# Kernel tuning notes

Hardware: AMD Instinct MI355X
Metric: run time of the kernel (lower is better)

Reference implementation:

```python
import jax, jax.numpy as jnp
import numpy as np

HEADS = 12
DIM_HEAD = 64
INNER = HEADS * DIM_HEAD  # 768
DIM = 512
KS = 3


def setup_inputs() -> dict:
    key = jax.random.key(0)
    ks = jax.random.split(key, 5)
    B, H, W = 8, 32, 32
    N = H * W + 1  # +1 cls token -> has_cls path
    x = jax.random.normal(ks[0], (B, N, DIM), dtype=jnp.float32)
    w_qkv = jax.random.normal(ks[1], (3 * INNER, DIM), dtype=jnp.float32) * (DIM ** -0.5)
    w_dw = jax.random.normal(ks[2], (DIM, 1, KS, KS), dtype=jnp.float32) * (1.0 / KS)
    w_out = jax.random.normal(ks[3], (DIM, INNER), dtype=jnp.float32) * (INNER ** -0.5)
    b_out = jax.random.normal(ks[4], (DIM,), dtype=jnp.float32) * 0.01
    return {"x": x, "w_qkv": w_qkv, "w_dw": w_dw, "w_out": w_out,
            "b_out": b_out, "h_feat": H, "w_feat": W}


def reference(x, w_qkv, w_dw, w_out, b_out, h_feat, w_feat):
    B, N, C = x.shape
    scale = DIM_HEAD ** -0.5
    # qkv projection (Linear, no bias): torch weight layout (out,in)
    qkv = jnp.einsum('bnc,oc->bno', x, w_qkv)  # (B,N,3*INNER)
    q, k, v = jnp.split(qkv, 3, axis=-1)

    def split_heads(t):
        return t.reshape(B, N, HEADS, DIM_HEAD).transpose(0, 2, 1, 3)  # (B,H,N,d)

    q, k, v = map(split_heads, (q, k, v))
    dots = jnp.einsum('bhid,bhjd->bhij', q, k) * scale
    attn = jax.nn.softmax(dots, axis=-1)
    out_attn = jnp.einsum('bhij,bhjd->bhid', attn, v)
    out_attn = out_attn.transpose(0, 2, 1, 3).reshape(B, N, INNER)

    has_cls = (N == h_feat * w_feat + 1)  # static
    spatial = x[:, 1:, :] if has_cls else x
    spatial_2d = spatial.transpose(0, 2, 1).reshape(B, C, h_feat, w_feat)
    # depthwise conv, padding = ks//2 (SAME for odd ks, stride 1)
    loc = jax.lax.conv_general_dilated(
        spatial_2d, w_dw, window_strides=(1, 1), padding='SAME',
        feature_group_count=C,
        dimension_numbers=('NCHW', 'OIHW', 'NCHW'))
    local_out = loc.reshape(B, C, h_feat * w_feat).transpose(0, 2, 1)  # (B,hw,C)
    if has_cls:
        cls_out = x[:, :1, :INNER]  # C < INNER so this is the full cls token
        local_out = jnp.concatenate([cls_out, local_out], axis=1)  # (B,N,C)
    if local_out.shape[-1] < INNER:
        out = out_attn + jnp.pad(
            local_out, ((0, 0), (0, 0), (0, INNER - local_out.shape[-1])))
    else:
        out = out_attn
    # output Linear (dropout=0 in eval)
    return jnp.einsum('bni,oi->bno', out, w_out) + b_out
```

## Files before the change

### kernel.cpp

```cpp
#include <hip/hip_runtime.h>
#include <hip/hip_bf16.h>
#include <stdint.h>
#include <math.h>

typedef __bf16 bf16;
typedef __bf16 bf16x8 __attribute__((ext_vector_type(8)));
typedef float f32x4 __attribute__((ext_vector_type(4)));

#define QSCALE 0.1803368801111f


__device__ __forceinline__ void gload_lds16(const void* g, void* l) {
  typedef const __attribute__((address_space(1))) char g_char;
  typedef __attribute__((address_space(3))) char l_char;
  g_char* gp = (g_char*)(uintptr_t)g;
  l_char* lp = (l_char*)(uint32_t)(uintptr_t)l;
  __builtin_amdgcn_global_load_lds(gp, lp, 16, 0, 0);
}

__device__ __forceinline__ float fexp2(float x) {
#if __has_builtin(__builtin_amdgcn_exp2f)
  return __builtin_amdgcn_exp2f(x);
#else
  return exp2f(x);
#endif
}

__device__ __forceinline__ float frcp(float x) {
#if __has_builtin(__builtin_amdgcn_rcpf)
  return __builtin_amdgcn_rcpf(x);
#else
  return 1.f / x;
#endif
}

__device__ __forceinline__ uint32_t pk2(float a, float b) {
  union { bf16 h; unsigned short u; } ua, ub;
  ua.h = (bf16)a; ub.h = (bf16)b;
  return (uint32_t)ua.u | ((uint32_t)ub.u << 16);
}

__global__ __launch_bounds__(256) void k_prep(const float* __restrict__ x,
                                              const float* __restrict__ wqkv,
                                              const float* __restrict__ wout,
                                              bf16* __restrict__ xb, bf16* __restrict__ wqkvb,
                                              bf16* __restrict__ woutb, bf16* __restrict__ vT) {
  int i = blockIdx.x * 256 + threadIdx.x;
  const float* src = nullptr;
  bf16* dst = nullptr;
  int q = i;
  bool zero = false;
  if (i < 1064960) {
    if (i < 1049600) src = x; else zero = true;
    dst = xb;
  } else if (i < 1064960 + 294912) {
    q = i - 1064960; src = wqkv; dst = wqkvb;
  } else if (i < 1064960 + 294912 + 98304) {
    q = i - (1064960 + 294912); src = wout; dst = woutb;
  } else {
    int qq = i - (1064960 + 294912 + 98304);
    int e = qq * 4;
    int rd = e >> 6;
    int n = 1024 + (e & 63);
    uint2 z; z.x = 0u; z.y = 0u;
    *(uint2*)&vT[(size_t)rd * 1088 + n] = z;
    return;
  }
  float4 v = make_float4(0.f, 0.f, 0.f, 0.f);
  if (!zero) v = *(const float4*)&src[(size_t)q * 4];
  uint2 p;
  p.x = pk2(v.x, v.y);
  p.y = pk2(v.z, v.w);
  *(uint2*)&dst[(size_t)q * 4] = p;
}

template <int EPI, int BN>
__global__ __launch_bounds__(256) void k_gemm(const bf16* __restrict__ A,
                                              const bf16* __restrict__ Bt, int K,
                                              bf16* __restrict__ q, bf16* __restrict__ kk,
                                              bf16* __restrict__ vt,
                                              const float* __restrict__ bias,
                                              float* __restrict__ out) {
  __shared__ __attribute__((aligned(16))) bf16 sA[128 * 64];
  __shared__ __attribute__((aligned(16))) bf16 sB[BN * 64];
  constexpr int MF = (BN == 128) ? 4 : 2;
  constexpr int WROWS = (BN == 128) ? 64 : 32;
  const int tid = threadIdx.x;
  const int lane = tid & 63;
  const int w = tid >> 6;
  const int wr = (BN == 128) ? (w >> 1) : w;
  const int wc = (BN == 128) ? (w & 1) : 0;
  const int tn = blockIdx.x, tm = blockIdx.y;
  const int l15 = lane & 15, l4 = lane >> 4;
  const int srow = lane >> 3, sslot = lane & 7;

  f32x4 acc[MF][4] = {};

  const int Ksteps = K >> 6;
  for (int kt = 0; kt < Ksteps; ++kt) {
    __syncthreads();
#pragma unroll
    for (int i = 0; i < 4; ++i) {
      int row = w * 32 + i * 8 + srow;
      int clog = sslot ^ (row & 7);
      gload_lds16(A + ((size_t)(tm * 128 + row) * K + kt * 64 + clog * 8),
                  &sA[(w * 32 + i * 8) * 64]);
    }
#pragma unroll
    for (int i = 0; i < BN / 32; ++i) {
      int row = w * (BN / 4) + i * 8 + srow;
      int clog = sslot ^ (row & 7);
      gload_lds16(Bt + ((size_t)(tn * BN + row) * K + kt * 64 + clog * 8),
                  &sB[(w * (BN / 4) + i * 8) * 64]);
    }
    __syncthreads();
#pragma unroll
    for (int ks = 0; ks < 2; ++ks) {
      bf16x8 af[MF], bfr[4];
#pragma unroll
      for (int mf = 0; mf < MF; ++mf) {
        int row = wr * WROWS + mf * 16 + l15;
        int phys = (ks * 4 + l4) ^ (row & 7);
        af[mf] = *(const bf16x8*)&sA[row * 64 + phys * 8];
      }
#pragma unroll
      for (int nf = 0; nf < 4; ++nf) {
        int row = wc * 64 + nf * 16 + l15;
        int phys = (ks * 4 + l4) ^ (row & 7);
        bfr[nf] = *(const bf16x8*)&sB[row * 64 + phys * 8];
      }
#pragma unroll
      for (int mf = 0; mf < MF; ++mf)
#pragma unroll
        for (int nf = 0; nf < 4; ++nf)
          acc[mf][nf] =
              __builtin_amdgcn_mfma_f32_16x16x32_bf16(af[mf], bfr[nf], acc[mf][nf], 0, 0, 0);
    }
  }

  const int Rbase = tm * 128 + wr * WROWS + l4 * 4;
  const int Cbase = tn * BN + wc * 64 + l15;
#pragma unroll
  for (int mf = 0; mf < MF; ++mf) {
    int R0 = Rbase + mf * 16;
    if (R0 >= 8200) continue;
    if (EPI == 0) {
      int b = R0 / 1025;
      int n0 = R0 - b * 1025;
      bool sb = (n0 + 3 <= 1024);
#pragma unroll
      for (int nf = 0; nf < 4; ++nf) {
        int Cc = Cbase + nf * 16;
        int seg = (Cc >= 1536) ? 2 : (Cc >= 768 ? 1 : 0);
        int inner = Cc - seg * 768;
        int h = inner >> 6, d = inner & 63;
        if (seg == 2) {
          if (sb) {
            uint2 p;
            p.x = pk2(acc[mf][nf][0], acc[mf][nf][1]);
            p.y = pk2(acc[mf][nf][2], acc[mf][nf][3]);
            *(uint2*)&vt[(((size_t)b * 12 + h) * 64 + d) * 1088 + n0] = p;
          } else {
#pragma unroll
            for (int r = 0; r < 4; ++r) {
              int R = R0 + r;
              int b2 = R / 1025;
              int n = R - b2 * 1025;
              vt[(((size_t)b2 * 12 + h) * 64 + d) * 1088 + n] = (bf16)acc[mf][nf][r];
            }
          }
        } else {
          bf16* dst = seg ? kk : q;
          float scl = seg ? 1.f : QSCALE;
#pragma unroll
          for (int r = 0; r < 4; ++r) {
            int b2, n;
            if (sb) { b2 = b; n = n0 + r; }
            else { int R = R0 + r; b2 = R / 1025; n = R - b2 * 1025; }
            dst[(((size_t)b2 * 12 + h) * 1088 + n) * 64 + d] = (bf16)(acc[mf][nf][r] * scl);
          }
        }
      }
    } else {
#pragma unroll
      for (int r = 0; r < 4; ++r) {
        int R = R0 + r;
#pragma unroll
        for (int nf = 0; nf < 4; ++nf) {
          int Cc = Cbase + nf * 16;
          out[(size_t)R * 512 + Cc] = acc[mf][nf][r] + bias[Cc];
        }
      }
    }
  }
}

__global__ __launch_bounds__(256) void k_flash(const bf16* __restrict__ qg,
                                               const bf16* __restrict__ kg,
                                               const bf16* __restrict__ vtg,
                                               bf16* __restrict__ outb) {
  __shared__ __attribute__((aligned(16))) bf16 sK[2][64 * 64];
  __shared__ __attribute__((aligned(16))) bf16 sV[2][64 * 64];
  __shared__ __attribute__((aligned(16))) bf16 sP[4][16 * 64];
  const int tid = threadIdx.x, lane = tid & 63, w = tid >> 6;
  const int l15 = lane & 15, l4 = lane >> 4;
  const int wg = blockIdx.x;
  const int logical = (wg & 7) * 108 + (wg >> 3);
  const int bh = logical / 9, qgp = logical - bh * 9;
  const int b = bh / 12, h = bh - b * 12;
  const int srow = lane >> 3, sslot = lane & 7;
  const int nsub = (qgp == 8) ? 1 : 2;
  const int swz = (l15 & 7) << 3;

  bf16x8 qf[2][2];
#pragma unroll
  for (int s = 0; s < 2; ++s) {
    if (s < nsub) {
      size_t qoff = ((size_t)bh * 1088 + (qgp * 2 + s) * 64 + w * 16 + l15) * 64 + l4 * 8;
      qf[s][0] = *(const bf16x8*)&qg[qoff];
      qf[s][1] = *(const bf16x8*)&qg[qoff + 32];
    }
  }

  float mreg[2] = {-INFINITY, -INFINITY};
  float lreg[2] = {0.f, 0.f};
  f32x4 oa[2][4] = {};

  const int px0 = (l4 ^ (l15 & 7)) * 8;
  const int px1 = ((4 + l4) ^ (l15 & 7)) * 8;
  const int stRow = (w * 16 + srow) * 64;
  const int stRow2 = (w * 16 + 8 + srow) * 64;

  auto STAGE = [&](int bi, int t) {
    int row = w * 16 + srow;
    int clog = sslot ^ (row & 7);
    gload_lds16(kg + ((size_t)bh * 1088 + t * 64 + row) * 64 + clog * 8, &sK[bi][stRow]);
    gload_lds16(vtg + ((size_t)bh * 64 + row) * 1088 + t * 64 + clog * 8, &sV[bi][stRow]);
    int row2 = row + 8;
    int clog2 = sslot ^ (row2 & 7);
    gload_lds16(kg + ((size_t)bh * 1088 + t * 64 + row2) * 64 + clog2 * 8, &sK[bi][stRow2]);
    gload_lds16(vtg + ((size_t)bh * 64 + row2) * 1088 + t * 64 + clog2 * 8, &sV[bi][stRow2]);
  };

  STAGE(0, 0);
  int cur = 0;

  for (int t = 0; t < 17; ++t) {
    asm volatile("s_waitcnt vmcnt(0)" ::: "memory");
    __builtin_amdgcn_s_barrier();
    __builtin_amdgcn_sched_barrier(0);
    if (t < 16) STAGE(cur ^ 1, t + 1);

    const bf16* kb_ = sK[cur];
    const bf16* vb_ = sV[cur];

    bf16x8 af[2][4], vf[2][4];
#pragma unroll
    for (int jt = 0; jt < 4; ++jt) {
      af[0][jt] = *(const bf16x8*)&kb_[(jt * 16 + l15) * 64 + px0];
      af[1][jt] = *(const bf16x8*)&kb_[(jt * 16 + l15) * 64 + px1];
      vf[0][jt] = *(const bf16x8*)&vb_[(jt * 16 + l15) * 64 + px0];
      vf[1][jt] = *(const bf16x8*)&vb_[(jt * 16 + l15) * 64 + px1];
    }

#pragma unroll
    for (int s = 0; s < 2; ++s) {
      if (s >= nsub) continue;
      f32x4 sc[4] = {};
      __builtin_amdgcn_s_setprio(1);
#pragma unroll
      for (int ks = 0; ks < 2; ++ks)
#pragma unroll
        for (int jt = 0; jt < 4; ++jt)
          sc[jt] = __builtin_amdgcn_mfma_f32_16x16x32_bf16(af[ks][jt], qf[s][ks], sc[jt], 0, 0, 0);
      __builtin_amdgcn_s_setprio(0);

      if (t == 16) {
#pragma unroll
        for (int jt = 0; jt < 4; ++jt)
#pragma unroll
          for (int r = 0; r < 4; ++r) {
            if (jt == 0 && r == 0)
              sc[jt][r] = (l4 == 0) ? sc[jt][r] : -INFINITY;
            else
              sc[jt][r] = -INFINITY;
          }
      }

      float pm = fmaxf(fmaxf(fmaxf(sc[0][0], sc[0][1]), fmaxf(sc[0][2], sc[0][3])),
                       fmaxf(fmaxf(sc[1][0], sc[1][1]), fmaxf(sc[1][2], sc[1][3])));
      float pm2 = fmaxf(fmaxf(fmaxf(sc[2][0], sc[2][1]), fmaxf(sc[2][2], sc[2][3])),
                        fmaxf(fmaxf(sc[3][0], sc[3][1]), fmaxf(sc[3][2], sc[3][3])));
      pm = fmaxf(pm, pm2);
      pm = fmaxf(pm, __shfl_xor(pm, 16));
      pm = fmaxf(pm, __shfl_xor(pm, 32));

      if (__any(pm > mreg[s] + 8.0f)) {
        float mn = fmaxf(mreg[s], pm);
        float alpha = fexp2(mreg[s] - mn);
        mreg[s] = mn;
        lreg[s] *= alpha;
        float ar[4];
#pragma unroll
        for (int r = 0; r < 4; ++r) ar[r] = __shfl(alpha, l4 * 4 + r);
#pragma unroll
        for (int db = 0; db < 4; ++db)
#pragma unroll
          for (int r = 0; r < 4; ++r) oa[s][db][r] *= ar[r];
      }
      float mn = mreg[s];

      float rs = 0.f;
#pragma unroll
      for (int jt = 0; jt < 4; ++jt) {
        float p0 = fexp2(sc[jt][0] - mn);
        float p1 = fexp2(sc[jt][1] - mn);
        float p2 = fexp2(sc[jt][2] - mn);
        float p3 = fexp2(sc[jt][3] - mn);
        rs += (p0 + p1) + (p2 + p3);
        uint2 pkd;
        pkd.x = pk2(p0, p1);
        pkd.y = pk2(p2, p3);
        *(uint2*)&sP[w][l15 * 64 + ((jt * 16 + l4 * 4) ^ swz)] = pkd;
      }
      rs += __shfl_xor(rs, 16);
      rs += __shfl_xor(rs, 32);
      lreg[s] += rs;

      __builtin_amdgcn_s_setprio(1);
#pragma unroll
      for (int ks = 0; ks < 2; ++ks) {
        bf16x8 pf = *(const bf16x8*)&sP[w][l15 * 64 + ((ks * 32 + l4 * 8) ^ swz)];
#pragma unroll
        for (int db = 0; db < 4; ++db)
          oa[s][db] = __builtin_amdgcn_mfma_f32_16x16x32_bf16(pf, vf[ks][db], oa[s][db], 0, 0, 0);
      }
      __builtin_amdgcn_s_setprio(0);
    }
    cur ^= 1;
  }

#pragma unroll
  for (int s = 0; s < 2; ++s) {
    if (s >= nsub) continue;
    float linv = frcp(lreg[s]);
#pragma unroll
    for (int r = 0; r < 4; ++r) {
      float ir = __shfl(linv, l4 * 4 + r);
      int n = (qgp * 2 + s) * 64 + w * 16 + l4 * 4 + r;
      if (n >= 1025) continue;
#pragma unroll
      for (int db = 0; db < 4; ++db)
        outb[((size_t)b * 1025 + n) * 768 + h * 64 + db * 16 + l15] = (bf16)(oa[s][db][r] * ir);
    }
  }
}

__global__ __launch_bounds__(256) void k_local(const float* __restrict__ x,
                                               const float* __restrict__ wdw,
                                               bf16* __restrict__ outb) {
  const int b = blockIdx.x, y = blockIdx.y, xseg = blockIdx.z, c0 = threadIdx.x;
  const int x0 = xseg * 8;
  const bool hm = (y > 0), hp = (y < 31);
#pragma unroll
  for (int hf = 0; hf < 2; ++hf) {
    const int c = hf * 256 + c0;
    float w9[9];
#pragma unroll
    for (int k = 0; k < 9; ++k) w9[k] = wdw[(size_t)c * 9 + k];
    const float* xb = x + ((size_t)b * 1025 + 1) * 512 + c;
    float A = 0.f, Bp = 0.f;
    for (int cc = x0 - 1; cc <= x0 + 8; ++cc) {
      float v0 = 0.f, v1 = 0.f, v2 = 0.f;
      if (cc >= 0 && cc < 32) {
        v1 = xb[((size_t)y * 32 + cc) * 512];
        if (hm) v0 = xb[((size_t)(y - 1) * 32 + cc) * 512];
        if (hp) v2 = xb[((size_t)(y + 1) * 32 + cc) * 512];
      }
      float t0 = v0 * w9[0] + v1 * w9[3] + v2 * w9[6];
      float t1 = v0 * w9[1] + v1 * w9[4] + v2 * w9[7];
      float t2 = v0 * w9[2] + v1 * w9[5] + v2 * w9[8];
      int oc = cc - 1;
      if (oc >= x0 && oc <= x0 + 7) {
        float acc = A + t2;
        size_t o = ((size_t)b * 1025 + 1 + y * 32 + oc) * 768 + c;
        outb[o] = (bf16)((float)outb[o] + acc);
      }
      A = Bp + t1;
      Bp = t0;
    }
  }
  if (y == 0 && xseg == 0) {
#pragma unroll
    for (int hf = 0; hf < 2; ++hf) {
      int c = hf * 256 + c0;
      size_t o = ((size_t)b * 1025) * 768 + c;
      outb[o] = (bf16)((float)outb[o] + x[((size_t)b * 1025) * 512 + c]);
    }
  }
}

extern "C" void kernel_launch(void* const* d_in, const int* in_sizes, int n_in,
                              void* d_out, int out_size, void* d_ws, size_t ws_size,
                              hipStream_t stream) {
  const float* x = (const float*)d_in[0];
  const float* w_qkv = (const float*)d_in[1];
  const float* w_dw = (const float*)d_in[2];
  const float* w_out = (const float*)d_in[3];
  const float* b_out = (const float*)d_in[4];
  float* out = (float*)d_out;

  char* ws = (char*)d_ws;
  size_t off = 0;
  auto alloc = [&](size_t bytes) {
    char* p = ws + off;
    off = (off + bytes + 255) & ~(size_t)255;
    return p;
  };
  bf16* xb    = (bf16*)alloc((size_t)8320 * 512 * 2);
  bf16* wqkvb = (bf16*)alloc((size_t)2304 * 512 * 2);
  bf16* woutb = (bf16*)alloc((size_t)512 * 768 * 2);
  bf16* qb    = (bf16*)alloc((size_t)96 * 1088 * 64 * 2);
  bf16* kb    = (bf16*)alloc((size_t)96 * 1088 * 64 * 2);
  bf16* vT    = (bf16*)alloc((size_t)96 * 64 * 1088 * 2);
  bf16* outb  = (bf16*)alloc((size_t)8320 * 768 * 2);

  k_prep<<<6080, 256, 0, stream>>>(x, w_qkv, w_out, xb, wqkvb, woutb, vT);
  k_gemm<0, 128><<<dim3(18, 65), 256, 0, stream>>>(xb, wqkvb, 512, qb, kb, vT, nullptr, nullptr);
  k_flash<<<864, 256, 0, stream>>>(qb, kb, vT, outb);
  k_local<<<dim3(8, 32, 4), 256, 0, stream>>>(x, w_dw, outb);
  k_gemm<1, 64><<<dim3(8, 65), 256, 0, stream>>>(outb, woutb, 768, nullptr, nullptr, nullptr,
                                                 b_out, out);
}
```

Baseline: 160.3 us.

## Redistribute softmax probabilities via lane shuffles instead of LDS round-trip

```diff
diff --git a/kernel.cpp b/kernel.cpp
--- a/kernel.cpp
+++ b/kernel.cpp
@@ -201,7 +201,6 @@
                                                bf16* __restrict__ outb) {
   __shared__ __attribute__((aligned(16))) bf16 sK[2][64 * 64];
   __shared__ __attribute__((aligned(16))) bf16 sV[2][64 * 64];
-  __shared__ __attribute__((aligned(16))) bf16 sP[4][16 * 64];
   const int tid = threadIdx.x, lane = tid & 63, w = tid >> 6;
   const int l15 = lane & 15, l4 = lane >> 4;
   const int wg = blockIdx.x;
@@ -210,7 +209,7 @@
   const int b = bh / 12, h = bh - b * 12;
   const int srow = lane >> 3, sslot = lane & 7;
   const int nsub = (qgp == 8) ? 1 : 2;
-  const int swz = (l15 & 7) << 3;
+  const int aa = l4 >> 1, bb = l4 & 1;
 
   bf16x8 qf[2][2];
 #pragma unroll
@@ -310,31 +309,49 @@
       }
       float mn = mreg[s];
 
-      float rs = 0.f;
-#pragma unroll
-      for (int jt = 0; jt < 4; ++jt) {
-        float p0 = fexp2(sc[jt][0] - mn);
-        float p1 = fexp2(sc[jt][1] - mn);
-        float p2 = fexp2(sc[jt][2] - mn);
-        float p3 = fexp2(sc[jt][3] - mn);
-        rs += (p0 + p1) + (p2 + p3);
-        uint2 pkd;
-        pkd.x = pk2(p0, p1);
-        pkd.y = pk2(p2, p3);
-        *(uint2*)&sP[w][l15 * 64 + ((jt * 16 + l4 * 4) ^ swz)] = pkd;
-      }
-      rs += __shfl_xor(rs, 16);
-      rs += __shfl_xor(rs, 32);
-      lreg[s] += rs;
+      uint32_t pk0u0, pk0u1, pk1u0, pk1u1, pk2u0, pk2u1, pk3u0, pk3u1;
+      float lsum = 0.f;
+      {
+        float p0, p1, p2, p3;
+        p0 = fexp2(sc[0][0] - mn); p1 = fexp2(sc[0][1] - mn);
+        p2 = fexp2(sc[0][2] - mn); p3 = fexp2(sc[0][3] - mn);
+        lsum += (p0 + p1) + (p2 + p3); pk0u0 = pk2(p0, p1); pk0u1 = pk2(p2, p3);
+        p0 = fexp2(sc[1][0] - mn); p1 = fexp2(sc[1][1] - mn);
+        p2 = fexp2(sc[1][2] - mn); p3 = fexp2(sc[1][3] - mn);
+        lsum += (p0 + p1) + (p2 + p3); pk1u0 = pk2(p0, p1); pk1u1 = pk2(p2, p3);
+        p0 = fexp2(sc[2][0] - mn); p1 = fexp2(sc[2][1] - mn);
+        p2 = fexp2(sc[2][2] - mn); p3 = fexp2(sc[2][3] - mn);
+        lsum += (p0 + p1) + (p2 + p3); pk2u0 = pk2(p0, p1); pk2u1 = pk2(p2, p3);
+        p0 = fexp2(sc[3][0] - mn); p1 = fexp2(sc[3][1] - mn);
+        p2 = fexp2(sc[3][2] - mn); p3 = fexp2(sc[3][3] - mn);
+        lsum += (p0 + p1) + (p2 + p3); pk3u0 = pk2(p0, p1); pk3u1 = pk2(p2, p3);
+      }
+      lreg[s] += lsum;
+
+      uint32_t O0 = aa ? pk1u0 : pk0u0, O1 = aa ? pk1u1 : pk0u1;
+      uint32_t O2 = aa ? pk3u0 : pk2u0, O3 = aa ? pk3u1 : pk2u1;
+      uint32_t S0 = aa ? pk0u0 : pk1u0, S1 = aa ? pk0u1 : pk1u1;
+      uint32_t S2 = aa ? pk2u0 : pk3u0, S3 = aa ? pk2u1 : pk3u1;
+      uint32_t R0 = (uint32_t)__shfl_xor((int)S0, 32), R1 = (uint32_t)__shfl_xor((int)S1, 32);
+      uint32_t R2 = (uint32_t)__shfl_xor((int)S2, 32), R3 = (uint32_t)__shfl_xor((int)S3, 32);
+      const int ab = aa ^ bb;
+      uint32_t U0 = ab ? O0 : R0, U1 = ab ? O1 : R1, U2 = ab ? O2 : R2, U3 = ab ? O3 : R3;
+      uint32_t K0 = ab ? R0 : O0, K1 = ab ? R1 : O1, K2 = ab ? R2 : O2, K3 = ab ? R3 : O3;
+      uint32_t T0 = (uint32_t)__shfl_xor((int)U0, 16), T1 = (uint32_t)__shfl_xor((int)U1, 16);
+      uint32_t T2 = (uint32_t)__shfl_xor((int)U2, 16), T3 = (uint32_t)__shfl_xor((int)U3, 16);
+      union { uint32_t u[4]; bf16x8 v; } pf0, pf1;
+      pf0.u[0] = bb ? T0 : K0; pf0.u[1] = bb ? T1 : K1;
+      pf0.u[2] = bb ? K0 : T0; pf0.u[3] = bb ? K1 : T1;
+      pf1.u[0] = bb ? T2 : K2; pf1.u[1] = bb ? T3 : K3;
+      pf1.u[2] = bb ? K2 : T2; pf1.u[3] = bb ? K3 : T3;
 
       __builtin_amdgcn_s_setprio(1);
 #pragma unroll
-      for (int ks = 0; ks < 2; ++ks) {
-        bf16x8 pf = *(const bf16x8*)&sP[w][l15 * 64 + ((ks * 32 + l4 * 8) ^ swz)];
-#pragma unroll
-        for (int db = 0; db < 4; ++db)
-          oa[s][db] = __builtin_amdgcn_mfma_f32_16x16x32_bf16(pf, vf[ks][db], oa[s][db], 0, 0, 0);
-      }
+      for (int db = 0; db < 4; ++db)
+        oa[s][db] = __builtin_amdgcn_mfma_f32_16x16x32_bf16(pf0.v, vf[0][db], oa[s][db], 0, 0, 0);
+#pragma unroll
+      for (int db = 0; db < 4; ++db)
+        oa[s][db] = __builtin_amdgcn_mfma_f32_16x16x32_bf16(pf1.v, vf[1][db], oa[s][db], 0, 0, 0);
       __builtin_amdgcn_s_setprio(0);
     }
     cur ^= 1;
@@ -343,7 +360,10 @@
 #pragma unroll
   for (int s = 0; s < 2; ++s) {
     if (s >= nsub) continue;
-    float linv = frcp(lreg[s]);
+    float ls = lreg[s];
+    ls += __shfl_xor(ls, 16);
+    ls += __shfl_xor(ls, 32);
+    float linv = frcp(ls);
 #pragma unroll
     for (int r = 0; r < 4; ++r) {
       float ir = __shfl(linv, l4 * 4 + r);
```

Measured after the change: 163.8 us. +2.2%, slower.

## Keep attention probabilities in registers via packed V layout and 16x16x16 MFMA

Applied to the files above, without the earlier changes.

```diff
diff --git a/kernel.cpp b/kernel.cpp
--- a/kernel.cpp
+++ b/kernel.cpp
@@ -6,6 +6,7 @@
 typedef __bf16 bf16;
 typedef __bf16 bf16x8 __attribute__((ext_vector_type(8)));
 typedef float f32x4 __attribute__((ext_vector_type(4)));
+typedef short s4 __attribute__((ext_vector_type(4)));
 
 #define QSCALE 0.1803368801111f
 
@@ -40,11 +41,20 @@
   return (uint32_t)ua.u | ((uint32_t)ub.u << 16);
 }
 
+__device__ __forceinline__ f32x4 pv_mfma(s4 a, s4 b, f32x4 c) {
+#if __has_builtin(__builtin_amdgcn_mfma_f32_16x16x16bf16_1k)
+  return __builtin_amdgcn_mfma_f32_16x16x16bf16_1k(a, b, c, 0, 0, 0);
+#else
+  asm volatile("v_mfma_f32_16x16x16_bf16 %0, %1, %2, %0" : "+v"(c) : "v"(a), "v"(b));
+  return c;
+#endif
+}
+
 __global__ __launch_bounds__(256) void k_prep(const float* __restrict__ x,
                                               const float* __restrict__ wqkv,
                                               const float* __restrict__ wout,
                                               bf16* __restrict__ xb, bf16* __restrict__ wqkvb,
-                                              bf16* __restrict__ woutb, bf16* __restrict__ vT) {
+                                              bf16* __restrict__ woutb, bf16* __restrict__ vP) {
   int i = blockIdx.x * 256 + threadIdx.x;
   const float* src = nullptr;
   bf16* dst = nullptr;
@@ -59,11 +69,11 @@
     q = i - (1064960 + 294912); src = wout; dst = woutb;
   } else {
     int qq = i - (1064960 + 294912 + 98304);
-    int e = qq * 4;
-    int rd = e >> 6;
-    int n = 1024 + (e & 63);
-    uint2 z; z.x = 0u; z.y = 0u;
-    *(uint2*)&vT[(size_t)rd * 1088 + n] = z;
+    int z = qq * 4;
+    int head = z >> 12;
+    int off = z & 4095;
+    uint2 zz; zz.x = 0u; zz.y = 0u;
+    *(uint2*)&vP[(size_t)head * 69632 + 65536 + off] = zz;
     return;
   }
   float4 v = make_float4(0.f, 0.f, 0.f, 0.f);
@@ -148,6 +158,7 @@
       int b = R0 / 1025;
       int n0 = R0 - b * 1025;
       bool sb = (n0 + 3 <= 1024);
+      bool sbv = sb && ((n0 & 3) == 0);
 #pragma unroll
       for (int nf = 0; nf < 4; ++nf) {
         int Cc = Cbase + nf * 16;
@@ -155,18 +166,19 @@
         int inner = Cc - seg * 768;
         int h = inner >> 6, d = inner & 63;
         if (seg == 2) {
-          if (sb) {
+          if (sbv) {
             uint2 p;
             p.x = pk2(acc[mf][nf][0], acc[mf][nf][1]);
             p.y = pk2(acc[mf][nf][2], acc[mf][nf][3]);
-            *(uint2*)&vt[(((size_t)b * 12 + h) * 64 + d) * 1088 + n0] = p;
+            *(uint2*)&vt[(((size_t)(b * 12 + h) * 272 + (n0 >> 2)) * 64 + d) * 4] = p;
           } else {
 #pragma unroll
             for (int r = 0; r < 4; ++r) {
               int R = R0 + r;
               int b2 = R / 1025;
               int n = R - b2 * 1025;
-              vt[(((size_t)b2 * 12 + h) * 64 + d) * 1088 + n] = (bf16)acc[mf][nf][r];
+              vt[(((size_t)(b2 * 12 + h) * 272 + (n >> 2)) * 64 + d) * 4 + (n & 3)] =
+                  (bf16)acc[mf][nf][r];
             }
           }
         } else {
@@ -197,11 +209,10 @@
 
 __global__ __launch_bounds__(256) void k_flash(const bf16* __restrict__ qg,
                                                const bf16* __restrict__ kg,
-                                               const bf16* __restrict__ vtg,
+                                               const bf16* __restrict__ vpg,
                                                bf16* __restrict__ outb) {
   __shared__ __attribute__((aligned(16))) bf16 sK[2][64 * 64];
-  __shared__ __attribute__((aligned(16))) bf16 sV[2][64 * 64];
-  __shared__ __attribute__((aligned(16))) bf16 sP[4][16 * 64];
+  __shared__ __attribute__((aligned(16))) bf16 sVP[2][16 * 256];
   const int tid = threadIdx.x, lane = tid & 63, w = tid >> 6;
   const int l15 = lane & 15, l4 = lane >> 4;
   const int wg = blockIdx.x;
@@ -210,7 +221,6 @@
   const int b = bh / 12, h = bh - b * 12;
   const int srow = lane >> 3, sslot = lane & 7;
   const int nsub = (qgp == 8) ? 1 : 2;
-  const int swz = (l15 & 7) << 3;
 
   bf16x8 qf[2][2];
 #pragma unroll
@@ -228,18 +238,18 @@
 
   const int px0 = (l4 ^ (l15 & 7)) * 8;
   const int px1 = ((4 + l4) ^ (l15 & 7)) * 8;
-  const int stRow = (w * 16 + srow) * 64;
-  const int stRow2 = (w * 16 + 8 + srow) * 64;
 
   auto STAGE = [&](int bi, int t) {
     int row = w * 16 + srow;
     int clog = sslot ^ (row & 7);
-    gload_lds16(kg + ((size_t)bh * 1088 + t * 64 + row) * 64 + clog * 8, &sK[bi][stRow]);
-    gload_lds16(vtg + ((size_t)bh * 64 + row) * 1088 + t * 64 + clog * 8, &sV[bi][stRow]);
+    gload_lds16(kg + ((size_t)bh * 1088 + t * 64 + row) * 64 + clog * 8, &sK[bi][row * 64]);
     int row2 = row + 8;
     int clog2 = sslot ^ (row2 & 7);
-    gload_lds16(kg + ((size_t)bh * 1088 + t * 64 + row2) * 64 + clog2 * 8, &sK[bi][stRow2]);
-    gload_lds16(vtg + ((size_t)bh * 64 + row2) * 1088 + t * 64 + clog2 * 8, &sV[bi][stRow2]);
+    gload_lds16(kg + ((size_t)bh * 1088 + t * 64 + row2) * 64 + clog2 * 8, &sK[bi][row2 * 64]);
+    size_t eb = (size_t)bh * 69632 + (size_t)t * 4096;
+    int lo = w * 1024 + lane * 8;
+    gload_lds16(vpg + eb + lo, &sVP[bi][lo]);
+    gload_lds16(vpg + eb + 512 + lo, &sVP[bi][512 + lo]);
   };
 
   STAGE(0, 0);
@@ -252,15 +262,17 @@
     if (t < 16) STAGE(cur ^ 1, t + 1);
 
     const bf16* kb_ = sK[cur];
-    const bf16* vb_ = sV[cur];
-
-    bf16x8 af[2][4], vf[2][4];
+    const bf16* vpb = sVP[cur];
+
+    bf16x8 af[2][4];
+    s4 vfr[4][4];
 #pragma unroll
     for (int jt = 0; jt < 4; ++jt) {
       af[0][jt] = *(const bf16x8*)&kb_[(jt * 16 + l15) * 64 + px0];
       af[1][jt] = *(const bf16x8*)&kb_[(jt * 16 + l15) * 64 + px1];
-      vf[0][jt] = *(const bf16x8*)&vb_[(jt * 16 + l15) * 64 + px0];
-      vf[1][jt] = *(const bf16x8*)&vb_[(jt * 16 + l15) * 64 + px1];
+#pragma unroll
+      for (int db = 0; db < 4; ++db)
+        vfr[jt][db] = *(const s4*)&vpb[((jt * 4 + l4) * 64 + db * 16 + l15) * 4];
     }
 
 #pragma unroll
@@ -310,31 +322,26 @@
       }
       float mn = mreg[s];
 
-      float rs = 0.f;
+      union { uint32_t u[2]; s4 v; } pa[4];
+      float lsum = 0.f;
 #pragma unroll
       for (int jt = 0; jt < 4; ++jt) {
         float p0 = fexp2(sc[jt][0] - mn);
         float p1 = fexp2(sc[jt][1] - mn);
         float p2 = fexp2(sc[jt][2] - mn);
         float p3 = fexp2(sc[jt][3] - mn);
-        rs += (p0 + p1) + (p2 + p3);
-        uint2 pkd;
-        pkd.x = pk2(p0, p1);
-        pkd.y = pk2(p2, p3);
-        *(uint2*)&sP[w][l15 * 64 + ((jt * 16 + l4 * 4) ^ swz)] = pkd;
-      }
-      rs += __shfl_xor(rs, 16);
-      rs += __shfl_xor(rs, 32);
-      lreg[s] += rs;
+        lsum += (p0 + p1) + (p2 + p3);
+        pa[jt].u[0] = pk2(p0, p1);
+        pa[jt].u[1] = pk2(p2, p3);
+      }
+      lreg[s] += lsum;
 
       __builtin_amdgcn_s_setprio(1);
 #pragma unroll
-      for (int ks = 0; ks < 2; ++ks) {
-        bf16x8 pf = *(const bf16x8*)&sP[w][l15 * 64 + ((ks * 32 + l4 * 8) ^ swz)];
+      for (int jt = 0; jt < 4; ++jt)
 #pragma unroll
         for (int db = 0; db < 4; ++db)
-          oa[s][db] = __builtin_amdgcn_mfma_f32_16x16x32_bf16(pf, vf[ks][db], oa[s][db], 0, 0, 0);
-      }
+          oa[s][db] = pv_mfma(pa[jt].v, vfr[jt][db], oa[s][db]);
       __builtin_amdgcn_s_setprio(0);
     }
     cur ^= 1;
@@ -343,7 +350,10 @@
 #pragma unroll
   for (int s = 0; s < 2; ++s) {
     if (s >= nsub) continue;
-    float linv = frcp(lreg[s]);
+    float ls = lreg[s];
+    ls += __shfl_xor(ls, 16);
+    ls += __shfl_xor(ls, 32);
+    float linv = frcp(ls);
 #pragma unroll
     for (int r = 0; r < 4; ++r) {
       float ir = __shfl(linv, l4 * 4 + r);
@@ -422,12 +432,12 @@
   bf16* woutb = (bf16*)alloc((size_t)512 * 768 * 2);
   bf16* qb    = (bf16*)alloc((size_t)96 * 1088 * 64 * 2);
   bf16* kb    = (bf16*)alloc((size_t)96 * 1088 * 64 * 2);
-  bf16* vT    = (bf16*)alloc((size_t)96 * 64 * 1088 * 2);
+  bf16* vP    = (bf16*)alloc((size_t)96 * 272 * 64 * 4 * 2);
   bf16* outb  = (bf16*)alloc((size_t)8320 * 768 * 2);
 
-  k_prep<<<6080, 256, 0, stream>>>(x, w_qkv, w_out, xb, wqkvb, woutb, vT);
-  k_gemm<0, 128><<<dim3(18, 65), 256, 0, stream>>>(xb, wqkvb, 512, qb, kb, vT, nullptr, nullptr);
-  k_flash<<<864, 256, 0, stream>>>(qb, kb, vT, outb);
+  k_prep<<<6080, 256, 0, stream>>>(x, w_qkv, w_out, xb, wqkvb, woutb, vP);
+  k_gemm<0, 128><<<dim3(18, 65), 256, 0, stream>>>(xb, wqkvb, 512, qb, kb, vP, nullptr, nullptr);
+  k_flash<<<864, 256, 0, stream>>>(qb, kb, vP, outb);
   k_local<<<dim3(8, 32, 4), 256, 0, stream>>>(x, w_dw, outb);
   k_gemm<1, 64><<<dim3(8, 65), 256, 0, stream>>>(outb, woutb, 768, nullptr, nullptr, nullptr,
                                                  b_out, out);
```

Measured after the change: 158.2 us. No clear change (-1.3%).
